# Optimization experiments

Measured on AMD Instinct MI355X. Metric: run time of the kernel, lower is better.

## Reference

```python
import jax, jax.numpy as jnp
import numpy as np

B, C, L, M, F, N = 4, 32, 256, 256, 8, 64  # N = L // 4 per build()


def setup_inputs() -> dict:
    key = jax.random.key(0)
    k1, k2, k3, k4 = jax.random.split(key, 4)
    return {
        "x_real": jax.random.normal(k1, (B, 1, C, L, M), dtype=jnp.float32),
        "x_imag": jax.random.normal(k2, (B, 1, C, L, M), dtype=jnp.float32),
        "w_real": jax.random.normal(k3, (F, C, N, 1), dtype=jnp.float32),
        "w_imag": jax.random.normal(k4, (F, C, N, 1), dtype=jnp.float32),
    }


def _interp_weights(w, L):
    """tfp.math.interp_regular_1d_grid along axis=-2: map x_targ=0..L-1 over
    ref range [0, L-1] onto an N-point regular grid, linear interpolation."""
    Nn = w.shape[-2]
    t = jnp.arange(L, dtype=jnp.float32) / (L - 1) * (Nn - 1)  # grid coords
    lo = jnp.clip(jnp.floor(t).astype(jnp.int32), 0, Nn - 2)
    frac = (t - lo.astype(jnp.float32))[:, None]               # (L, 1)
    return w[:, :, lo, :] * (1.0 - frac) + w[:, :, lo + 1, :] * frac  # (F,C,L,1)


def reference(x_real, x_imag, w_real, w_imag):
    Lm = x_real.shape[-2]
    wr = _interp_weights(w_real, Lm)  # (F, C, L, 1)
    wi = _interp_weights(w_imag, Lm)
    # complex multiply: (wr + i*wi) * (xr + i*xi), broadcast (B,1,C,L,M)->(B,F,C,L,M)
    pr = wr * x_real - wi * x_imag
    pi = wr * x_imag + wi * x_real
    scale = jnp.sqrt(1.0 + jnp.arange(Lm, dtype=jnp.float32))[:, None]  # self.l, (L,1)
    yr = jnp.mean(pr, axis=-3) * scale  # (B, F, L, M)
    yi = jnp.mean(pi, axis=-3) * scale
    yr = jax.nn.relu(yr)  # relu=True: relu applied to real part only
    return jnp.stack([yr, yi])  # (2, B, F, L, M) == (real, imag)
```

## Files before the change

kernel.cpp:

```cpp
#include <hip/hip_runtime.h>
#include <math.h>

constexpr int B_ = 4, C_ = 32, L_ = 256, M_ = 256, F_ = 8, N_ = 64;

__global__ __launch_bounds__(256) void sphereconv_kernel(
    const float* __restrict__ xr, const float* __restrict__ xi,
    const float* __restrict__ wr, const float* __restrict__ wi,
    float* __restrict__ out)
{
    __shared__ float4 ws_r[C_ * 2];
    __shared__ float4 ws_i[C_ * 2];

    const int b = blockIdx.x / L_;
    const int l = blockIdx.x % L_;
    const int m = threadIdx.x;

    const float t = ((float)l / (float)(L_ - 1)) * (float)(N_ - 1);
    int lo = (int)floorf(t);
    if (lo > N_ - 2) lo = N_ - 2;
    const float frac = t - (float)lo;

    {
        const int idx = threadIdx.x;
        const int c = idx >> 3, f = idx & 7;
        const int base = (f * C_ + c) * N_ + lo;
        ((float*)ws_r)[c * F_ + f] = wr[base] * (1.0f - frac) + wr[base + 1] * frac;
        ((float*)ws_i)[c * F_ + f] = wi[base] * (1.0f - frac) + wi[base + 1] * frac;
    }
    __syncthreads();

    float4 ar = {0.f,0.f,0.f,0.f}, br = {0.f,0.f,0.f,0.f};
    float4 ai = {0.f,0.f,0.f,0.f}, bi = {0.f,0.f,0.f,0.f};

    const size_t strideC = (size_t)L_ * M_;
    const size_t xoff = (size_t)b * C_ * strideC + (size_t)l * M_ + m;
    const float* xrp = xr + xoff;
    const float* xip = xi + xoff;

#pragma unroll 8
    for (int c = 0; c < C_; ++c) {
        const float vr = xrp[(size_t)c * strideC];
        const float vi = xip[(size_t)c * strideC];
        const float4 w0 = ws_r[c * 2 + 0];
        const float4 w1 = ws_r[c * 2 + 1];
        const float4 u0 = ws_i[c * 2 + 0];
        const float4 u1 = ws_i[c * 2 + 1];
        ar.x += w0.x * vr - u0.x * vi;  ai.x += w0.x * vi + u0.x * vr;
        ar.y += w0.y * vr - u0.y * vi;  ai.y += w0.y * vi + u0.y * vr;
        ar.z += w0.z * vr - u0.z * vi;  ai.z += w0.z * vi + u0.z * vr;
        ar.w += w0.w * vr - u0.w * vi;  ai.w += w0.w * vi + u0.w * vr;
        br.x += w1.x * vr - u1.x * vi;  bi.x += w1.x * vi + u1.x * vr;
        br.y += w1.y * vr - u1.y * vi;  bi.y += w1.y * vi + u1.y * vr;
        br.z += w1.z * vr - u1.z * vi;  bi.z += w1.z * vi + u1.z * vr;
        br.w += w1.w * vr - u1.w * vi;  bi.w += w1.w * vi + u1.w * vr;
    }

    const float scale = sqrtf(1.0f + (float)l) * (1.0f / (float)C_);
    const float accr[F_] = {ar.x, ar.y, ar.z, ar.w, br.x, br.y, br.z, br.w};
    const float acci[F_] = {ai.x, ai.y, ai.z, ai.w, bi.x, bi.y, bi.z, bi.w};

    const size_t o0 = (((size_t)b * F_) * L_ + l) * M_ + m;
    const size_t imagOff = (size_t)B_ * F_ * L_ * M_;
#pragma unroll
    for (int f = 0; f < F_; ++f) {
        float yr = accr[f] * scale;
        yr = fmaxf(yr, 0.0f);
        const float yi = acci[f] * scale;
        out[o0 + (size_t)f * strideC] = yr;
        out[o0 + (size_t)f * strideC + imagOff] = yi;
    }
}

extern "C" void kernel_launch(void* const* d_in, const int* in_sizes, int n_in,
                              void* d_out, int out_size, void* d_ws, size_t ws_size,
                              hipStream_t stream) {
    const float* xr = (const float*)d_in[0];
    const float* xi = (const float*)d_in[1];
    const float* wr = (const float*)d_in[2];
    const float* wi = (const float*)d_in[3];
    float* out = (float*)d_out;
    sphereconv_kernel<<<dim3(B_ * L_), dim3(256), 0, stream>>>(xr, xi, wr, wi, out);
}
```

Before: 120.8 us.

## Vectorize x loads and output stores with float4, one wave per block

Each thread now handles four consecutive m positions, using float4 global loads of x and float4 stores of the outputs. The block shrinks to a single 64-thread wavefront, and each thread computes eight interpolated weights into a merged shared array. The goal is fewer, wider memory instructions on a bandwidth-bound kernel. In exchange each thread keeps 64 accumulators, which raises register pressure, and with only 1024 one-wave blocks there is less latency hiding per CU.

```diff
diff --git a/kernel.cpp b/kernel.cpp
--- a/kernel.cpp
+++ b/kernel.cpp
@@ -3,71 +3,83 @@
 
 constexpr int B_ = 4, C_ = 32, L_ = 256, M_ = 256, F_ = 8, N_ = 64;
 
-__global__ __launch_bounds__(256) void sphereconv_kernel(
+__global__ __launch_bounds__(64) void sphereconv_kernel(
     const float* __restrict__ xr, const float* __restrict__ xi,
     const float* __restrict__ wr, const float* __restrict__ wi,
     float* __restrict__ out)
 {
-    __shared__ float4 ws_r[C_ * 2];
-    __shared__ float4 ws_i[C_ * 2];
+    __shared__ float ws[C_ * 16];
 
-    const int b = blockIdx.x / L_;
-    const int l = blockIdx.x % L_;
-    const int m = threadIdx.x;
+    const int b    = blockIdx.x >> 8;
+    const int l    = blockIdx.x & (L_ - 1);
+    const int lane = threadIdx.x;
 
     const float t = ((float)l / (float)(L_ - 1)) * (float)(N_ - 1);
     int lo = (int)floorf(t);
     if (lo > N_ - 2) lo = N_ - 2;
     const float frac = t - (float)lo;
 
-    {
-        const int idx = threadIdx.x;
-        const int c = idx >> 3, f = idx & 7;
+#pragma unroll
+    for (int i = 0; i < 8; ++i) {
+        const int idx = lane * 8 + i;
+        const int c   = idx >> 4;
+        const int j   = idx & 15;
+        const int f   = j & 7;
+        const float* w = (j & 8) ? wi : wr;
         const int base = (f * C_ + c) * N_ + lo;
-        ((float*)ws_r)[c * F_ + f] = wr[base] * (1.0f - frac) + wr[base + 1] * frac;
-        ((float*)ws_i)[c * F_ + f] = wi[base] * (1.0f - frac) + wi[base + 1] * frac;
+        ws[c * 16 + j] = w[base] * (1.0f - frac) + w[base + 1] * frac;
     }
     __syncthreads();
 
-    float4 ar = {0.f,0.f,0.f,0.f}, br = {0.f,0.f,0.f,0.f};
-    float4 ai = {0.f,0.f,0.f,0.f}, bi = {0.f,0.f,0.f,0.f};
+    float4 accr[F_], acci[F_];
+#pragma unroll
+    for (int f = 0; f < F_; ++f) {
+        accr[f] = make_float4(0.f, 0.f, 0.f, 0.f);
+        acci[f] = make_float4(0.f, 0.f, 0.f, 0.f);
+    }
 
-    const size_t strideC = (size_t)L_ * M_;
-    const size_t xoff = (size_t)b * C_ * strideC + (size_t)l * M_ + m;
-    const float* xrp = xr + xoff;
-    const float* xip = xi + xoff;
+    const size_t strideC4 = (size_t)L_ * M_ / 4;
+    const size_t xoff = ((size_t)b * C_) * L_ * M_ + (size_t)l * M_ + lane * 4;
+    const float4* xr4 = (const float4*)(xr + xoff);
+    const float4* xi4 = (const float4*)(xi + xoff);
 
-#pragma unroll 8
+#pragma unroll 4
     for (int c = 0; c < C_; ++c) {
-        const float vr = xrp[(size_t)c * strideC];
-        const float vi = xip[(size_t)c * strideC];
-        const float4 w0 = ws_r[c * 2 + 0];
-        const float4 w1 = ws_r[c * 2 + 1];
-        const float4 u0 = ws_i[c * 2 + 0];
-        const float4 u1 = ws_i[c * 2 + 1];
-        ar.x += w0.x * vr - u0.x * vi;  ai.x += w0.x * vi + u0.x * vr;
-        ar.y += w0.y * vr - u0.y * vi;  ai.y += w0.y * vi + u0.y * vr;
-        ar.z += w0.z * vr - u0.z * vi;  ai.z += w0.z * vi + u0.z * vr;
-        ar.w += w0.w * vr - u0.w * vi;  ai.w += w0.w * vi + u0.w * vr;
-        br.x += w1.x * vr - u1.x * vi;  bi.x += w1.x * vi + u1.x * vr;
-        br.y += w1.y * vr - u1.y * vi;  bi.y += w1.y * vi + u1.y * vr;
-        br.z += w1.z * vr - u1.z * vi;  bi.z += w1.z * vi + u1.z * vr;
-        br.w += w1.w * vr - u1.w * vi;  bi.w += w1.w * vi + u1.w * vr;
+        const float4 vr = xr4[c * strideC4];
+        const float4 vi = xi4[c * strideC4];
+        const float4 w0 = *(const float4*)&ws[c * 16 + 0];
+        const float4 w1 = *(const float4*)&ws[c * 16 + 4];
+        const float4 u0 = *(const float4*)&ws[c * 16 + 8];
+        const float4 u1 = *(const float4*)&ws[c * 16 + 12];
+        const float wrf[8] = {w0.x, w0.y, w0.z, w0.w, w1.x, w1.y, w1.z, w1.w};
+        const float wif[8] = {u0.x, u0.y, u0.z, u0.w, u1.x, u1.y, u1.z, u1.w};
+#pragma unroll
+        for (int f = 0; f < F_; ++f) {
+            const float a = wrf[f], bb = wif[f];
+            accr[f].x += a * vr.x - bb * vi.x;  acci[f].x += a * vi.x + bb * vr.x;
+            accr[f].y += a * vr.y - bb * vi.y;  acci[f].y += a * vi.y + bb * vr.y;
+            accr[f].z += a * vr.z - bb * vi.z;  acci[f].z += a * vi.z + bb * vr.z;
+            accr[f].w += a * vr.w - bb * vi.w;  acci[f].w += a * vi.w + bb * vr.w;
+        }
     }
 
     const float scale = sqrtf(1.0f + (float)l) * (1.0f / (float)C_);
-    const float accr[F_] = {ar.x, ar.y, ar.z, ar.w, br.x, br.y, br.z, br.w};
-    const float acci[F_] = {ai.x, ai.y, ai.z, ai.w, bi.x, bi.y, bi.z, bi.w};
-
-    const size_t o0 = (((size_t)b * F_) * L_ + l) * M_ + m;
+    const size_t o0      = (((size_t)b * F_) * L_ + l) * M_ + lane * 4;
     const size_t imagOff = (size_t)B_ * F_ * L_ * M_;
+    const size_t fStride = (size_t)L_ * M_;
 #pragma unroll
     for (int f = 0; f < F_; ++f) {
-        float yr = accr[f] * scale;
-        yr = fmaxf(yr, 0.0f);
-        const float yi = acci[f] * scale;
-        out[o0 + (size_t)f * strideC] = yr;
-        out[o0 + (size_t)f * strideC + imagOff] = yi;
+        float4 yr, yi;
+        yr.x = fmaxf(accr[f].x * scale, 0.f);
+        yr.y = fmaxf(accr[f].y * scale, 0.f);
+        yr.z = fmaxf(accr[f].z * scale, 0.f);
+        yr.w = fmaxf(accr[f].w * scale, 0.f);
+        yi.x = acci[f].x * scale;
+        yi.y = acci[f].y * scale;
+        yi.z = acci[f].z * scale;
+        yi.w = acci[f].w * scale;
+        *(float4*)(out + o0 + (size_t)f * fStride)           = yr;
+        *(float4*)(out + o0 + (size_t)f * fStride + imagOff) = yi;
     }
 }
 
@@ -79,5 +91,5 @@
     const float* wr = (const float*)d_in[2];
     const float* wi = (const float*)d_in[3];
     float* out = (float*)d_out;
-    sphereconv_kernel<<<dim3(B_ * L_), dim3(256), 0, stream>>>(xr, xi, wr, wi, out);
+    sphereconv_kernel<<<dim3(B_ * L_), dim3(64), 0, stream>>>(xr, xi, wr, wi, out);
 }
```

Result: slower. 127.4 us (+5.5%).
